# Optimization experiments

Measured on AMD Instinct MI355X. Metric: run time of the kernel, lower is better.

Reference implementation:

```python
import jax, jax.numpy as jnp
import numpy as np

B, N, H, ITERS = 4, 4096, 128, 8
EPS = 1e-5  # torch LayerNorm default


def _mlp(x, w1, b1, w2, b2, w3, b3):
    x = jax.nn.relu(x @ w1.T + b1)
    x = jax.nn.relu(x @ w2.T + b2)
    return x @ w3.T + b3


def setup_inputs() -> dict:
    key = jax.random.key(0)
    ks = jax.random.split(key, 16)
    s = 0.05
    nrm = lambda k, shape: jax.random.normal(k, shape, jnp.float32) * s
    z = lambda *shape: jnp.zeros(shape, jnp.float32)
    return {
        "x": jax.random.normal(ks[0], (B, N, N), jnp.float32),
        "k": jax.random.uniform(ks[1], (B,), jnp.float32, 1.0, 10.0),
        "n": jax.random.uniform(ks[2], (B,), jnp.float32, 10.0, 100.0),
        "mask": (jax.random.uniform(ks[3], (B, N)) < 0.9).astype(jnp.float32),
        # init MLP: 2 -> H -> H -> H (torch Linear convention: [out, in])
        "init_w1": nrm(ks[4], (H, 2)), "init_b1": z(H),
        "init_w2": nrm(ks[5], (H, H)), "init_b2": z(H),
        "init_w3": nrm(ks[6], (H, H)), "init_b3": z(H),
        # msg MLP: H -> H -> H -> H
        "msg_w1": nrm(ks[7], (H, H)), "msg_b1": z(H),
        "msg_w2": nrm(ks[8], (H, H)), "msg_b2": z(H),
        "msg_w3": nrm(ks[9], (H, H)), "msg_b3": z(H),
        # LSTMCell (gate order i, f, g, o)
        "lstm_wih": nrm(ks[10], (4 * H, H)), "lstm_whh": nrm(ks[11], (4 * H, H)),
        "lstm_bih": z(4 * H), "lstm_bhh": z(4 * H),
        # LayerNorm affine
        "ln_g": jnp.ones(H, jnp.float32), "ln_b": z(H),
        # vote MLP: H -> H -> H -> 1
        "vote_w1": nrm(ks[12], (H, H)), "vote_b1": z(H),
        "vote_w2": nrm(ks[13], (H, H)), "vote_b2": z(H),
        "vote_w3": nrm(ks[14], (1, H)), "vote_b3": z(1),
    }


def reference(x, k, n, mask,
              init_w1, init_b1, init_w2, init_b2, init_w3, init_b3,
              msg_w1, msg_b1, msg_w2, msg_b2, msg_w3, msg_b3,
              lstm_wih, lstm_whh, lstm_bih, lstm_bhh,
              ln_g, ln_b,
              vote_w1, vote_b1, vote_w2, vote_b2, vote_w3, vote_b3):
    b, n_node, _ = x.shape

    def ln(h):
        mu = h.mean(-1, keepdims=True)
        xc = h - mu
        var = (xc * xc).mean(-1, keepdims=True)
        return xc * jax.lax.rsqrt(var + EPS) * ln_g + ln_b

    nk = jnp.stack([k, n], axis=1)                          # [B, 2]
    init0 = _mlp(nk, init_w1, init_b1, init_w2, init_b2, init_w3, init_b3)
    h = jnp.broadcast_to(init0[:, None, :], (b, n_node, init0.shape[-1]))  # [B, N, H]
    c = jnp.zeros_like(h)
    embed = ln(h)
    for _ in range(ITERS):
        m = _mlp(embed, msg_w1, msg_b1, msg_w2, msg_b2, msg_w3, msg_b3)   # [B, N, H]
        msg = jnp.einsum('bij,bjh->bih', x, m)                            # dense aggregation
        gates = msg @ lstm_wih.T + lstm_bih + h @ lstm_whh.T + lstm_bhh   # [B, N, 4H]
        i, f, g, o = jnp.split(gates, 4, axis=-1)
        c = jax.nn.sigmoid(f) * c + jax.nn.sigmoid(i) * jnp.tanh(g)
        h = jax.nn.sigmoid(o) * jnp.tanh(c)
        embed = ln(h)
    vote = _mlp(embed, vote_w1, vote_b1, vote_w2, vote_b2, vote_w3, vote_b3)[..., 0]  # [B, N]
    return jax.nn.sigmoid((vote * mask).sum(axis=1))        # [B]
```

## Files before the change

kernel.cpp:

```cpp
#include <hip/hip_runtime.h>
#include <cstddef>
#include <cstdint>

#define LN_EPS 1e-5f

typedef __attribute__((ext_vector_type(8))) short bf16x8;
typedef __attribute__((ext_vector_type(4))) float f32x4;

__device__ __forceinline__ unsigned short f2bf(float f) {
    unsigned u = __float_as_uint(f);
    u += 0x7FFFu + ((u >> 16) & 1u);
    return (unsigned short)(u >> 16);
}
__device__ __forceinline__ float bf2f(unsigned short s) {
    return __uint_as_float(((unsigned)s) << 16);
}
__device__ __forceinline__ float sigf(float x) { return 1.f / (1.f + __expf(-x)); }

__device__ __forceinline__ void gload_lds16(const void* g, void* l) {
    __builtin_amdgcn_global_load_lds(
        (const __attribute__((address_space(1))) unsigned int*)(unsigned long long)(uintptr_t)g,
        (__attribute__((address_space(3))) unsigned int*)(unsigned int)(uintptr_t)l,
        16, 0, 0);
}

__device__ __forceinline__ void layer128(const unsigned short* __restrict__ W,
                                         const bf16x8 a[4], f32x4 acc[8],
                                         int lr, int lq)
{
#pragma unroll
    for (int s = 0; s < 4; ++s) {
#pragma unroll
        for (int tn = 0; tn < 8; ++tn) {
            bf16x8 b = *(const bf16x8*)(W + (tn * 16 + lr) * 128 + s * 32 + lq * 8);
            acc[tn] = __builtin_amdgcn_mfma_f32_16x16x32_bf16(a[s], b, acc[tn], 0, 0, 0);
        }
    }
}

template<bool FP8>
__global__ __launch_bounds__(256)
void msg_mlp_kernel(const unsigned short* __restrict__ embed,
                    const unsigned short* __restrict__ w1, const float* __restrict__ b1,
                    const unsigned short* __restrict__ w2, const float* __restrict__ b2,
                    const unsigned short* __restrict__ w3, const float* __restrict__ b3,
                    unsigned short* __restrict__ m_t, unsigned char* __restrict__ m8,
                    int N)
{
    __shared__ unsigned short sact[4][16][136];
    const int lane = threadIdx.x & 63, wave = threadIdx.x >> 6;
    const int lr = lane & 15, lq = lane >> 4;
    const int r0 = (blockIdx.x * 4 + wave) * 16;

    bf16x8 a[4];
    f32x4 acc[8];

#pragma unroll
    for (int s = 0; s < 4; ++s)
        a[s] = *(const bf16x8*)(embed + (long long)(r0 + lr) * 128 + s * 32 + lq * 8);
#pragma unroll
    for (int tn = 0; tn < 8; ++tn) acc[tn] = (f32x4)(0.f);
    layer128(w1, a, acc, lr, lq);

#pragma unroll
    for (int tn = 0; tn < 8; ++tn) {
        float bb = b1[tn * 16 + lr];
#pragma unroll
        for (int r = 0; r < 4; ++r) {
            float v = acc[tn][r] + bb; v = v > 0.f ? v : 0.f;
            sact[wave][lq * 4 + r][tn * 16 + lr] = f2bf(v);
        }
    }
    __syncthreads();
#pragma unroll
    for (int s = 0; s < 4; ++s)
        a[s] = *(const bf16x8*)&sact[wave][lr][s * 32 + lq * 8];
#pragma unroll
    for (int tn = 0; tn < 8; ++tn) acc[tn] = (f32x4)(0.f);
    layer128(w2, a, acc, lr, lq);

#pragma unroll
    for (int tn = 0; tn < 8; ++tn) {
        float bb = b2[tn * 16 + lr];
#pragma unroll
        for (int r = 0; r < 4; ++r) {
            float v = acc[tn][r] + bb; v = v > 0.f ? v : 0.f;
            sact[wave][lq * 4 + r][tn * 16 + lr] = f2bf(v);
        }
    }
    __syncthreads();
#pragma unroll
    for (int s = 0; s < 4; ++s)
        a[s] = *(const bf16x8*)&sact[wave][lr][s * 32 + lq * 8];
#pragma unroll
    for (int tn = 0; tn < 8; ++tn) acc[tn] = (f32x4)(0.f);
    layer128(w3, a, acc, lr, lq);

    const int batch = r0 / N;
    const int rin0 = r0 - batch * N + lq * 4;
#pragma unroll
    for (int tn = 0; tn < 8; ++tn) {
        float bb = b3[tn * 16 + lr];
        float v0 = acc[tn][0] + bb, v1 = acc[tn][1] + bb;
        float v2 = acc[tn][2] + bb, v3 = acc[tn][3] + bb;
        if constexpr (FP8) {
            int pk = __builtin_amdgcn_cvt_pk_fp8_f32(v0, v1, 0, false);
            pk = __builtin_amdgcn_cvt_pk_fp8_f32(v2, v3, pk, true);
            *(unsigned int*)(m8 + (long long)(batch * 128 + tn * 16 + lr) * N + rin0) = (unsigned)pk;
        } else {
            ushort4 o;
            o.x = f2bf(v0); o.y = f2bf(v1); o.z = f2bf(v2); o.w = f2bf(v3);
            *(ushort4*)(m_t + ((long long)(batch * 128 + tn * 16 + lr)) * N + rin0) = o;
        }
    }
}

__global__ __launch_bounds__(256)
void agg_fp8_kernel(const unsigned char* __restrict__ x8,
                    const unsigned char* __restrict__ m8,
                    unsigned short* __restrict__ msgp, int N, long long BNH)
{
    __shared__ unsigned char sA[2][128 * 128];
    __shared__ unsigned char sB[2][128 * 128];

    const int tid = threadIdx.x;
    const int lane = tid & 63, w = tid >> 6;
    const int lr = lane & 15, lq = lane >> 4;
    const int wr = w & 1, wc = w >> 1;
    const int r0 = blockIdx.x * 128;
    const int ksp = blockIdx.y;
    const int batch = blockIdx.z;
    const int kbase = ksp * (N >> 2);
    const int nsteps = (N >> 2) >> 7;

    const unsigned char* xrow = x8 + (long long)batch * N * N;
    const unsigned char* mrow = m8 + (long long)batch * 128 * N;

    f32x4 acc[4][4];
#pragma unroll
    for (int tr = 0; tr < 4; ++tr)
#pragma unroll
        for (int tn = 0; tn < 4; ++tn) acc[tr][tn] = (f32x4)(0.f);

    auto stage = [&](int b, int step) {
        const int k0 = kbase + step * 128;
#pragma unroll
        for (int j = 0; j < 4; ++j) {
            const int c = ((w * 4 + j) << 6) + lane;
            const int row = c >> 3;
            const int gs = (c & 7) ^ (row & 7);
            gload_lds16(xrow + (long long)(r0 + row) * N + k0 + gs * 16,
                        (char*)sA[b] + (w * 4 + j) * 1024);
        }
#pragma unroll
        for (int j = 0; j < 4; ++j) {
            const int c = ((w * 4 + j) << 6) + lane;
            const int row = c >> 3;
            const int gs = (c & 7) ^ (row & 7);
            gload_lds16(mrow + (long long)row * N + k0 + gs * 16,
                        (char*)sB[b] + (w * 4 + j) * 1024);
        }
    };

    stage(0, 0);
    __syncthreads();
    int buf = 0;
    for (int step = 0; step < nsteps; ++step) {
        if (step + 1 < nsteps) stage(buf ^ 1, step + 1);
        const unsigned char* A  = sA[buf];
        const unsigned char* Bp = sB[buf];
#pragma unroll
        for (int ks = 0; ks < 4; ++ks) {
            const int g    = ks * 4 + lq;
            const int half = (g & 1) << 3;
            const int s16  = g >> 1;
            long af[4], bfr[4];
#pragma unroll
            for (int tr = 0; tr < 4; ++tr) {
                const int row = wr * 64 + tr * 16 + lr;
                af[tr] = *(const long*)(A + row * 128 + ((s16 ^ (row & 7)) << 4) + half);
            }
#pragma unroll
            for (int tn = 0; tn < 4; ++tn) {
                const int row = wc * 64 + tn * 16 + lr;
                bfr[tn] = *(const long*)(Bp + row * 128 + ((s16 ^ (row & 7)) << 4) + half);
            }
#pragma unroll
            for (int tr = 0; tr < 4; ++tr)
#pragma unroll
                for (int tn = 0; tn < 4; ++tn)
                    acc[tr][tn] = __builtin_amdgcn_mfma_f32_16x16x32_fp8_fp8(
                        af[tr], bfr[tn], acc[tr][tn], 0, 0, 0);
        }
        __syncthreads();
        buf ^= 1;
    }

    unsigned short* outb = msgp + (long long)ksp * BNH + (long long)(batch * N + r0) * 128;
#pragma unroll
    for (int tr = 0; tr < 4; ++tr)
#pragma unroll
        for (int tn = 0; tn < 4; ++tn)
#pragma unroll
            for (int r = 0; r < 4; ++r)
                outb[(long long)(wr * 64 + tr * 16 + lq * 4 + r) * 128 + wc * 64 + tn * 16 + lr]
                    = f2bf(acc[tr][tn][r]);
}

__global__ __launch_bounds__(256)
void agg_fallback_kernel(const float* __restrict__ xf,
                         const unsigned short* __restrict__ mt, float* __restrict__ msgp0,
                         int N)
{
    __shared__ float sacc[4][16][132];
    const int lane = threadIdx.x & 63, wave = threadIdx.x >> 6;
    const int lr = lane & 15, lq = lane >> 4;
    const int batch = blockIdx.y;
    const int rowBase = blockIdx.x * 16;
    const int kBase = wave * (N >> 2);
    const int kIters = N >> 7;

    const float* af = xf + (long long)batch * N * N + (long long)(rowBase + lr) * N + kBase + lq * 8;
    const long long bbase = (long long)batch * 128 * N + (long long)lr * N + kBase + lq * 8;

    f32x4 acc[8];
#pragma unroll
    for (int tn = 0; tn < 8; ++tn) acc[tn] = (f32x4)(0.f);

    for (int it = 0; it < kIters; ++it) {
        const int k = it * 32;
        float4 lo = *(const float4*)(af + k);
        float4 hi = *(const float4*)(af + k + 4);
        bf16x8 a0;
        a0[0] = (short)f2bf(lo.x); a0[1] = (short)f2bf(lo.y);
        a0[2] = (short)f2bf(lo.z); a0[3] = (short)f2bf(lo.w);
        a0[4] = (short)f2bf(hi.x); a0[5] = (short)f2bf(hi.y);
        a0[6] = (short)f2bf(hi.z); a0[7] = (short)f2bf(hi.w);
#pragma unroll
        for (int tn = 0; tn < 8; ++tn) {
            bf16x8 b0 = *(const bf16x8*)(mt + bbase + (long long)tn * 16 * N + k);
            acc[tn] = __builtin_amdgcn_mfma_f32_16x16x32_bf16(a0, b0, acc[tn], 0, 0, 0);
        }
    }

#pragma unroll
    for (int tn = 0; tn < 8; ++tn)
#pragma unroll
        for (int r = 0; r < 4; ++r)
            sacc[wave][lq * 4 + r][tn * 16 + lr] = acc[tn][r];
    __syncthreads();
    {
        const int t = threadIdx.x;
        const int row = t >> 4, cb2 = (t & 15) * 8;
        float o[8];
#pragma unroll
        for (int j = 0; j < 8; ++j)
            o[j] = sacc[0][row][cb2 + j] + sacc[1][row][cb2 + j]
                 + sacc[2][row][cb2 + j] + sacc[3][row][cb2 + j];
        float* dst = msgp0 + (long long)(batch * N + rowBase + row) * 128 + cb2;
        *(float4*)dst = make_float4(o[0], o[1], o[2], o[3]);
        *(float4*)(dst + 4) = make_float4(o[4], o[5], o[6], o[7]);
    }
}

template<int NPART, bool BF16P>
__global__ __launch_bounds__(256)
void gates_lstm_kernel(const void* __restrict__ msgp, long long BNH,
                       unsigned short* hb, float* cb,
                       const unsigned short* __restrict__ wih,
                       const unsigned short* __restrict__ whh,
                       const float* __restrict__ bih, const float* __restrict__ bhh,
                       const float* __restrict__ lng, const float* __restrict__ lnb,
                       unsigned short* __restrict__ embed_out)
{
    __shared__ float sred[4][16][2];
    const int lane = threadIdx.x & 63, wave = threadIdx.x >> 6;
    const int lr = lane & 15, lq = lane >> 4;
    const int r0 = blockIdx.x * 16;

    f32x4 acc[8];
#pragma unroll
    for (int t = 0; t < 8; ++t) acc[t] = (f32x4)(0.f);

    bf16x8 a[4];
#pragma unroll
    for (int s = 0; s < 4; ++s) {
        const long long base = (long long)(r0 + lr) * 128 + s * 32 + lq * 8;
        float v[8];
        if constexpr (BF16P) {
            const unsigned short* mp = (const unsigned short*)msgp;
            bf16x8 t0 = *(const bf16x8*)(mp + base);
#pragma unroll
            for (int e = 0; e < 8; ++e) v[e] = bf2f((unsigned short)t0[e]);
#pragma unroll
            for (int j = 1; j < NPART; ++j) {
                bf16x8 tj = *(const bf16x8*)(mp + (long long)j * BNH + base);
#pragma unroll
                for (int e = 0; e < 8; ++e) v[e] += bf2f((unsigned short)tj[e]);
            }
        } else {
            const float* mp = (const float*)msgp;
            float4 t0 = *(const float4*)(mp + base);
            float4 t1 = *(const float4*)(mp + base + 4);
            v[0] = t0.x; v[1] = t0.y; v[2] = t0.z; v[3] = t0.w;
            v[4] = t1.x; v[5] = t1.y; v[6] = t1.z; v[7] = t1.w;
#pragma unroll
            for (int j = 1; j < NPART; ++j) {
                float4 u0 = *(const float4*)(mp + (long long)j * BNH + base);
                float4 u1 = *(const float4*)(mp + (long long)j * BNH + base + 4);
                v[0] += u0.x; v[1] += u0.y; v[2] += u0.z; v[3] += u0.w;
                v[4] += u1.x; v[5] += u1.y; v[6] += u1.z; v[7] += u1.w;
            }
        }
        bf16x8 r8;
#pragma unroll
        for (int e = 0; e < 8; ++e) r8[e] = (short)f2bf(v[e]);
        a[s] = r8;
    }
#pragma unroll
    for (int s = 0; s < 4; ++s)
#pragma unroll
        for (int tt = 0; tt < 8; ++tt) {
            const int brow = (tt >> 1) * 128 + wave * 32 + (tt & 1) * 16 + lr;
            bf16x8 b = *(const bf16x8*)(wih + brow * 128 + s * 32 + lq * 8);
            acc[tt] = __builtin_amdgcn_mfma_f32_16x16x32_bf16(a[s], b, acc[tt], 0, 0, 0);
        }
#pragma unroll
    for (int s = 0; s < 4; ++s)
        a[s] = *(const bf16x8*)((const unsigned short*)hb + (long long)(r0 + lr) * 128 + s * 32 + lq * 8);
#pragma unroll
    for (int s = 0; s < 4; ++s)
#pragma unroll
        for (int tt = 0; tt < 8; ++tt) {
            const int brow = (tt >> 1) * 128 + wave * 32 + (tt & 1) * 16 + lr;
            bf16x8 b = *(const bf16x8*)(whh + brow * 128 + s * 32 + lq * 8);
            acc[tt] = __builtin_amdgcn_mfma_f32_16x16x32_bf16(a[s], b, acc[tt], 0, 0, 0);
        }

    float hn[2][4];
    float4* cw = (float4*)cb;
#pragma unroll
    for (int half = 0; half < 2; ++half) {
        const int col = wave * 32 + half * 16 + lr;
        const float bi  = bih[col]       + bhh[col];
        const float bf_ = bih[col + 128] + bhh[col + 128];
        const float bg  = bih[col + 256] + bhh[col + 256];
        const float bo  = bih[col + 384] + bhh[col + 384];
        const long long cidx = ((long long)blockIdx.x * 8 + wave * 2 + half) * 64 + lane;
        float4 cold = cw[cidx];
        float co[4] = {cold.x, cold.y, cold.z, cold.w};
        float cn[4];
#pragma unroll
        for (int r = 0; r < 4; ++r) {
            float iv = acc[0 + half][r] + bi;
            float fv = acc[2 + half][r] + bf_;
            float gv = acc[4 + half][r] + bg;
            float ov = acc[6 + half][r] + bo;
            float cc = sigf(fv) * co[r] + sigf(iv) * tanhf(gv);
            cn[r] = cc;
            hn[half][r] = sigf(ov) * tanhf(cc);
        }
        float4 cnew = {cn[0], cn[1], cn[2], cn[3]};
        cw[cidx] = cnew;
    }

    float ps1[4], ps2[4];
#pragma unroll
    for (int r = 0; r < 4; ++r) {
        float s1 = hn[0][r] + hn[1][r];
        float s2 = hn[0][r] * hn[0][r] + hn[1][r] * hn[1][r];
#pragma unroll
        for (int m = 1; m <= 8; m <<= 1) {
            s1 += __shfl_xor(s1, m);
            s2 += __shfl_xor(s2, m);
        }
        ps1[r] = s1; ps2[r] = s2;
    }
    if (lr == 0) {
#pragma unroll
        for (int r = 0; r < 4; ++r) {
            sred[wave][lq * 4 + r][0] = ps1[r];
            sred[wave][lq * 4 + r][1] = ps2[r];
        }
    }
    __syncthreads();

#pragma unroll
    for (int half = 0; half < 2; ++half) {
        const int col = wave * 32 + half * 16 + lr;
        const float g = lng[col], bb = lnb[col];
#pragma unroll
        for (int r = 0; r < 4; ++r) {
            const int row = lq * 4 + r;
            float S1 = sred[0][row][0] + sred[1][row][0] + sred[2][row][0] + sred[3][row][0];
            float S2 = sred[0][row][1] + sred[1][row][1] + sred[2][row][1] + sred[3][row][1];
            float mean = S1 * (1.f / 128.f);
            float var  = S2 * (1.f / 128.f) - mean * mean;
            float rs = rsqrtf(var + LN_EPS);
            long long off = (long long)(r0 + row) * 128 + col;
            hb[off] = f2bf(hn[half][r]);
            embed_out[off] = f2bf((hn[half][r] - mean) * rs * g + bb);
        }
    }
}

__global__ __launch_bounds__(256)
void vote_mlp_kernel(const unsigned short* __restrict__ embed,
                     const unsigned short* __restrict__ w1, const float* __restrict__ b1,
                     const unsigned short* __restrict__ w2, const float* __restrict__ b2,
                     const float* __restrict__ w3, const float* __restrict__ b3p,
                     const float* __restrict__ mask, float* __restrict__ logit, int N)
{
    __shared__ unsigned short sact[4][16][136];
    const int lane = threadIdx.x & 63, wave = threadIdx.x >> 6;
    const int lr = lane & 15, lq = lane >> 4;
    const int r0 = (blockIdx.x * 4 + wave) * 16;

    bf16x8 a[4];
    f32x4 acc[8];
#pragma unroll
    for (int s = 0; s < 4; ++s)
        a[s] = *(const bf16x8*)(embed + (long long)(r0 + lr) * 128 + s * 32 + lq * 8);
#pragma unroll
    for (int tn = 0; tn < 8; ++tn) acc[tn] = (f32x4)(0.f);
    layer128(w1, a, acc, lr, lq);

#pragma unroll
    for (int tn = 0; tn < 8; ++tn) {
        float bb = b1[tn * 16 + lr];
#pragma unroll
        for (int r = 0; r < 4; ++r) {
            float v = acc[tn][r] + bb; v = v > 0.f ? v : 0.f;
            sact[wave][lq * 4 + r][tn * 16 + lr] = f2bf(v);
        }
    }
    __syncthreads();
#pragma unroll
    for (int s = 0; s < 4; ++s)
        a[s] = *(const bf16x8*)&sact[wave][lr][s * 32 + lq * 8];
#pragma unroll
    for (int tn = 0; tn < 8; ++tn) acc[tn] = (f32x4)(0.f);
    layer128(w2, a, acc, lr, lq);

    float dot[4] = {0.f, 0.f, 0.f, 0.f};
#pragma unroll
    for (int tn = 0; tn < 8; ++tn) {
        const int col = tn * 16 + lr;
        const float bb = b2[col], w3c = w3[col];
#pragma unroll
        for (int r = 0; r < 4; ++r) {
            float v = acc[tn][r] + bb; v = v > 0.f ? v : 0.f;
            dot[r] += v * w3c;
        }
    }
#pragma unroll
    for (int r = 0; r < 4; ++r)
#pragma unroll
        for (int m = 1; m <= 8; m <<= 1) dot[r] += __shfl_xor(dot[r], m);

    const int batch = r0 / N;
    const float b3 = b3p[0];
    const int base = r0 + lq * 4;
    float wsum = mask[base + 0] * (dot[0] + b3) + mask[base + 1] * (dot[1] + b3)
               + mask[base + 2] * (dot[2] + b3) + mask[base + 3] * (dot[3] + b3);
    float t = (lr == 0) ? wsum : 0.f;
    t += __shfl_xor(t, 16);
    t += __shfl_xor(t, 32);
    if (lane == 0) atomicAdd(&logit[batch], t);
}

__global__ __launch_bounds__(128)
void init_kernel(const float* __restrict__ kk, const float* __restrict__ nn,
                 const float* __restrict__ w1, const float* __restrict__ b1,
                 const float* __restrict__ w2, const float* __restrict__ b2,
                 const float* __restrict__ w3, const float* __restrict__ b3,
                 const float* __restrict__ lng, const float* __restrict__ lnb,
                 float* __restrict__ init0, float* __restrict__ embed0,
                 float* __restrict__ logit, int H)
{
    int b = blockIdx.x, j = threadIdx.x;
    __shared__ float s1[128];
    __shared__ float s2[128];
    __shared__ float red[128];
    if (j == 0) logit[b] = 0.f;
    float kv = kk[b], nv = nn[b];
    float h1 = w1[j * 2 + 0] * kv + w1[j * 2 + 1] * nv + b1[j];
    h1 = h1 > 0.f ? h1 : 0.f;
    s1[j] = h1; __syncthreads();
    float h2 = b2[j];
    for (int q = 0; q < H; ++q) h2 += w2[j * H + q] * s1[q];
    h2 = h2 > 0.f ? h2 : 0.f;
    s2[j] = h2; __syncthreads();
    float o = b3[j];
    for (int q = 0; q < H; ++q) o += w3[j * H + q] * s2[q];
    init0[b * H + j] = o;

    red[j] = o; __syncthreads();
    for (int s = 64; s > 0; s >>= 1) { if (j < s) red[j] += red[j + s]; __syncthreads(); }
    float mu = red[0] / (float)H;
    __syncthreads();
    float d = o - mu;
    red[j] = d * d; __syncthreads();
    for (int s = 64; s > 0; s >>= 1) { if (j < s) red[j] += red[j + s]; __syncthreads(); }
    float var = red[0] / (float)H;
    embed0[b * H + j] = d * rsqrtf(var + LN_EPS) * lng[j] + lnb[j];
}

__global__ void bcast_kernel(const float* __restrict__ init0, const float* __restrict__ embed0,
                             unsigned short* __restrict__ hb, float* __restrict__ cb,
                             unsigned short* __restrict__ embed,
                             long long total, long long NH)
{
    long long idx = (long long)blockIdx.x * blockDim.x + threadIdx.x;
    if (idx >= total) return;
    int b = (int)(idx / NH);
    int j = (int)(idx & 127);
    hb[idx] = f2bf(init0[b * 128 + j]);
    embed[idx] = f2bf(embed0[b * 128 + j]);
    cb[idx] = 0.f;
}

__global__ void cast8_kernel(const float* __restrict__ x, unsigned char* __restrict__ x8,
                             long long n8)
{
    long long i = ((long long)blockIdx.x * blockDim.x + threadIdx.x);
    if (i >= n8) return;
    const float* s = x + i * 8;
    float4 a = *(const float4*)s;
    float4 b = *(const float4*)(s + 4);
    int lo = __builtin_amdgcn_cvt_pk_fp8_f32(a.x, a.y, 0, false);
    lo = __builtin_amdgcn_cvt_pk_fp8_f32(a.z, a.w, lo, true);
    int hi = __builtin_amdgcn_cvt_pk_fp8_f32(b.x, b.y, 0, false);
    hi = __builtin_amdgcn_cvt_pk_fp8_f32(b.z, b.w, hi, true);
    int2 o; o.x = lo; o.y = hi;
    *(int2*)(x8 + i * 8) = o;
}

struct CastArgs {
    const float* src[7];
    unsigned short* dst[7];
    int n[7];
};

__global__ void castw_kernel(CastArgs a)
{
    int rg = blockIdx.y;
    int i = (blockIdx.x * blockDim.x + threadIdx.x) * 4;
    if (i < a.n[rg]) {
        float4 v = *(const float4*)(a.src[rg] + i);
        ushort4 o;
        o.x = f2bf(v.x); o.y = f2bf(v.y); o.z = f2bf(v.z); o.w = f2bf(v.w);
        *(ushort4*)(a.dst[rg] + i) = o;
    }
}

__global__ void sigmoid_kernel(const float* __restrict__ logit, float* __restrict__ out, int B)
{
    int b = threadIdx.x;
    if (b < B) out[b] = 1.f / (1.f + __expf(-logit[b]));
}

extern "C" void kernel_launch(void* const* d_in, const int* in_sizes, int n_in,
                              void* d_out, int out_size, void* d_ws, size_t ws_size,
                              hipStream_t stream)
{
    const float* x    = (const float*)d_in[0];
    const float* kk   = (const float*)d_in[1];
    const float* nn   = (const float*)d_in[2];
    const float* mask = (const float*)d_in[3];
    const float* iw1  = (const float*)d_in[4];
    const float* ib1  = (const float*)d_in[5];
    const float* iw2  = (const float*)d_in[6];
    const float* ib2  = (const float*)d_in[7];
    const float* iw3  = (const float*)d_in[8];
    const float* ib3  = (const float*)d_in[9];
    const float* mw1  = (const float*)d_in[10];
    const float* mb1  = (const float*)d_in[11];
    const float* mw2  = (const float*)d_in[12];
    const float* mb2  = (const float*)d_in[13];
    const float* mw3  = (const float*)d_in[14];
    const float* mb3  = (const float*)d_in[15];
    const float* wih  = (const float*)d_in[16];
    const float* whh  = (const float*)d_in[17];
    const float* bih  = (const float*)d_in[18];
    const float* bhh  = (const float*)d_in[19];
    const float* lng  = (const float*)d_in[20];
    const float* lnb  = (const float*)d_in[21];
    const float* vw1  = (const float*)d_in[22];
    const float* vb1  = (const float*)d_in[23];
    const float* vw2  = (const float*)d_in[24];
    const float* vb2  = (const float*)d_in[25];
    const float* vw3  = (const float*)d_in[26];
    const float* vb3  = (const float*)d_in[27];
    float* out = (float*)d_out;

    const int B = in_sizes[1];
    const int H = in_sizes[5];
    const int N = in_sizes[3] / B;
    const long long NH  = (long long)N * H;
    const long long BNH = (long long)B * NH;
    const int M = B * N;

    char* p = (char*)d_ws;
    auto alloc = [&](long long bytes) {
        char* q = p; p += (bytes + 255) & ~255LL; return q;
    };
    float*          cb     = (float*)alloc(BNH * 4);
    unsigned short* embed  = (unsigned short*)alloc(BNH * 2);
    unsigned short* hb     = (unsigned short*)alloc(BNH * 2);
    unsigned short* m_t    = (unsigned short*)alloc(BNH * 2);
    unsigned short* msgp   = (unsigned short*)alloc(4 * BNH * 2);
    float*          init0  = (float*)alloc((long long)B * H * 4);
    float*          embed0 = (float*)alloc((long long)B * H * 4);
    float*          logit  = (float*)alloc((long long)B * 4);
    unsigned short* wb_m1  = (unsigned short*)alloc((long long)H * H * 2);
    unsigned short* wb_m2  = (unsigned short*)alloc((long long)H * H * 2);
    unsigned short* wb_m3  = (unsigned short*)alloc((long long)H * H * 2);
    unsigned short* wb_ih  = (unsigned short*)alloc(4LL * H * H * 2);
    unsigned short* wb_hh  = (unsigned short*)alloc(4LL * H * H * 2);
    unsigned short* wb_v1  = (unsigned short*)alloc((long long)H * H * 2);
    unsigned short* wb_v2  = (unsigned short*)alloc((long long)H * H * 2);
    unsigned char*  m8_t   = (unsigned char*)alloc(BNH);
    unsigned char*  x8     = (unsigned char*)alloc((long long)B * N * N);
    const bool use_x8 = ((long long)(p - (char*)d_ws) <= (long long)ws_size);

    init_kernel<<<B, H, 0, stream>>>(kk, nn, iw1, ib1, iw2, ib2, iw3, ib3, lng, lnb,
                                     init0, embed0, logit, H);
    {
        long long nb = (BNH + 255) / 256;
        bcast_kernel<<<dim3((unsigned)nb), 256, 0, stream>>>(init0, embed0, hb, cb, embed, BNH, NH);
    }
    {
        CastArgs ca;
        ca.src[0] = mw1; ca.dst[0] = wb_m1; ca.n[0] = H * H;
        ca.src[1] = mw2; ca.dst[1] = wb_m2; ca.n[1] = H * H;
        ca.src[2] = mw3; ca.dst[2] = wb_m3; ca.n[2] = H * H;
        ca.src[3] = wih; ca.dst[3] = wb_ih; ca.n[3] = 4 * H * H;
        ca.src[4] = whh; ca.dst[4] = wb_hh; ca.n[4] = 4 * H * H;
        ca.src[5] = vw1; ca.dst[5] = wb_v1; ca.n[5] = H * H;
        ca.src[6] = vw2; ca.dst[6] = wb_v2; ca.n[6] = H * H;
        castw_kernel<<<dim3(64, 7), 256, 0, stream>>>(ca);
    }
    if (use_x8) {
        long long n8 = (long long)B * N * N / 8;
        cast8_kernel<<<dim3((unsigned)((n8 + 255) / 256)), 256, 0, stream>>>(x, x8, n8);
    }

    dim3 gridRow(M / 64);
    dim3 gridRow16(M / 16);
    dim3 gridAggNew(N / 128, 4, B);
    dim3 gridAggOld(N / 16, B);

    for (int it = 0; it < 8; ++it) {
        if (use_x8) {
            msg_mlp_kernel<true><<<gridRow, 256, 0, stream>>>(embed, wb_m1, mb1, wb_m2, mb2,
                                                              wb_m3, mb3, m_t, m8_t, N);
            agg_fp8_kernel<<<gridAggNew, 256, 0, stream>>>(x8, m8_t, msgp, N, BNH);
            gates_lstm_kernel<4, true><<<gridRow16, 256, 0, stream>>>(
                (const void*)msgp, BNH, hb, cb, wb_ih, wb_hh, bih, bhh, lng, lnb, embed);
        } else {
            msg_mlp_kernel<false><<<gridRow, 256, 0, stream>>>(embed, wb_m1, mb1, wb_m2, mb2,
                                                               wb_m3, mb3, m_t, m8_t, N);
            agg_fallback_kernel<<<gridAggOld, 256, 0, stream>>>(x, m_t, (float*)msgp, N);
            gates_lstm_kernel<1, false><<<gridRow16, 256, 0, stream>>>(
                (const void*)msgp, BNH, hb, cb, wb_ih, wb_hh, bih, bhh, lng, lnb, embed);
        }
    }

    vote_mlp_kernel<<<gridRow, 256, 0, stream>>>(embed, wb_v1, vb1, wb_v2, vb2,
                                                 vw3, vb3, mask, logit, N);
    sigmoid_kernel<<<1, 64, 0, stream>>>(logit, out, B);
}
```

Measured before the change: 1.135 ms.

## Fuse whole pipeline into one persistent cooperative kernel with grid syncs

Replaces the sequence of per-iteration kernel launches (msg MLP, fp8 aggregation, gates/LSTM, vote) with a single cooperative kernel of 512 blocks that runs all phases separated by grid-wide barriers. The message MLP is fused into the gates tile so the new embedding stays in shared memory instead of round-tripping through global memory. The vote MLP is fused into the final gates pass in the same way. This removes launch overhead and some intermediate traffic. In exchange the aggregation loses its double-buffered LDS prefetch, and each phase pays for grid sync costs.

```diff
diff --git a/kernel.cpp b/kernel.cpp
--- a/kernel.cpp
+++ b/kernel.cpp
@@ -1,8 +1,13 @@
 #include <hip/hip_runtime.h>
+#include <hip/hip_cooperative_groups.h>
 #include <cstddef>
 #include <cstdint>
 
+namespace cg = cooperative_groups;
+
 #define LN_EPS 1e-5f
+#define NB 512
+#define NT 256
 
 typedef __attribute__((ext_vector_type(8))) short bf16x8;
 typedef __attribute__((ext_vector_type(4))) float f32x4;
@@ -22,6 +27,537 @@
         (const __attribute__((address_space(1))) unsigned int*)(unsigned long long)(uintptr_t)g,
         (__attribute__((address_space(3))) unsigned int*)(unsigned int)(uintptr_t)l,
         16, 0, 0);
+}
+
+struct UberArgs {
+    const float *x, *kk, *nn, *mask;
+    const float *iw1, *ib1, *iw2, *ib2, *iw3, *ib3;
+    const float *mw1, *mb1, *mw2, *mb2, *mw3, *mb3;
+    const float *wih, *whh, *bih, *bhh, *lng, *lnb;
+    const float *vw1, *vb1, *vw2, *vb2, *vw3, *vb3;
+    unsigned short *wm1, *wm2, *wm3, *wih_b, *whh_b, *wv1, *wv2;
+    unsigned char *x8, *m8;
+    unsigned short *msgp;
+    unsigned short *hb;
+    float *cb;
+    float *init0, *embed0, *logit, *out;
+    int N, B, iters;
+    long long BNH;
+};
+
+__device__ void prologue(const UberArgs& A, char* smem)
+{
+    const int tid = threadIdx.x;
+    const long long gtid = (long long)blockIdx.x * NT + tid;
+    const long long GT = (long long)NB * NT;
+    const int N = A.N, B_ = A.B;
+
+    const long long n8 = (long long)B_ * N * N / 8;
+    for (long long i = gtid; i < n8; i += GT) {
+        const float* s = A.x + i * 8;
+        float4 a0 = *(const float4*)s;
+        float4 b0 = *(const float4*)(s + 4);
+        int lo = __builtin_amdgcn_cvt_pk_fp8_f32(a0.x, a0.y, 0, false);
+        lo = __builtin_amdgcn_cvt_pk_fp8_f32(a0.z, a0.w, lo, true);
+        int hi = __builtin_amdgcn_cvt_pk_fp8_f32(b0.x, b0.y, 0, false);
+        hi = __builtin_amdgcn_cvt_pk_fp8_f32(b0.z, b0.w, hi, true);
+        int2 o; o.x = lo; o.y = hi;
+        *(int2*)(A.x8 + i * 8) = o;
+    }
+    {
+        const float* srcs[7] = {A.mw1, A.mw2, A.mw3, A.wih, A.whh, A.vw1, A.vw2};
+        unsigned short* dsts[7] = {A.wm1, A.wm2, A.wm3, A.wih_b, A.whh_b, A.wv1, A.wv2};
+        const int ns[7] = {16384, 16384, 16384, 65536, 65536, 16384, 16384};
+        for (int rg = 0; rg < 7; ++rg) {
+            const float* s = srcs[rg]; unsigned short* d = dsts[rg];
+            const int n4 = ns[rg] >> 2;
+            for (long long i = gtid; i < n4; i += GT) {
+                float4 v = *(const float4*)(s + i * 4);
+                ushort4 o;
+                o.x = f2bf(v.x); o.y = f2bf(v.y); o.z = f2bf(v.z); o.w = f2bf(v.w);
+                *(ushort4*)(d + i * 4) = o;
+            }
+        }
+    }
+    const long long nc4 = A.BNH >> 2;
+    const float4 z4 = make_float4(0.f, 0.f, 0.f, 0.f);
+    for (long long i = gtid; i < nc4; i += GT) ((float4*)A.cb)[i] = z4;
+    if (blockIdx.x == 0 && tid < B_) A.logit[tid] = 0.f;
+
+    if ((int)blockIdx.x >= NB - B_) {
+        const int b = blockIdx.x - (NB - B_);
+        float* s1 = (float*)smem;
+        float* s2 = s1 + 128;
+        float* red = s2 + 128;
+        const bool act = tid < 128;
+        const int j = tid;
+        const float kv = A.kk[b], nv = A.nn[b];
+        float h1 = 0.f, h2 = 0.f, o = 0.f;
+        if (act) {
+            h1 = A.iw1[j * 2 + 0] * kv + A.iw1[j * 2 + 1] * nv + A.ib1[j];
+            h1 = h1 > 0.f ? h1 : 0.f;
+            s1[j] = h1;
+        }
+        __syncthreads();
+        if (act) {
+            h2 = A.ib2[j];
+            for (int q = 0; q < 128; ++q) h2 += A.iw2[j * 128 + q] * s1[q];
+            h2 = h2 > 0.f ? h2 : 0.f;
+            s2[j] = h2;
+        }
+        __syncthreads();
+        if (act) {
+            o = A.ib3[j];
+            for (int q = 0; q < 128; ++q) o += A.iw3[j * 128 + q] * s2[q];
+            A.init0[b * 128 + j] = o;
+            red[j] = o;
+        }
+        __syncthreads();
+        for (int s = 64; s > 0; s >>= 1) { if (tid < s) red[tid] += red[tid + s]; __syncthreads(); }
+        const float mu = red[0] * (1.f / 128.f);
+        __syncthreads();
+        if (act) red[j] = (o - mu) * (o - mu);
+        __syncthreads();
+        for (int s = 64; s > 0; s >>= 1) { if (tid < s) red[tid] += red[tid + s]; __syncthreads(); }
+        if (act) {
+            const float var = red[0] * (1.f / 128.f);
+            A.embed0[b * 128 + j] = (o - mu) * rsqrtf(var + LN_EPS) * A.lng[j] + A.lnb[j];
+        }
+    }
+}
+
+__device__ __forceinline__ void msg_tile(const UberArgs& A, int tile,
+                                         unsigned short (*ebt)[136], unsigned short (*act)[136])
+{
+    const int tid = threadIdx.x;
+    const int lane = tid & 63, wave = tid >> 6;
+    const int lr = lane & 15, lq = lane >> 4;
+    const int r0 = tile * 16;
+    const int N = A.N;
+    bf16x8 a[4];
+    f32x4 acc2[2];
+
+#pragma unroll
+    for (int s = 0; s < 4; ++s) a[s] = *(const bf16x8*)&ebt[lr][s * 32 + lq * 8];
+    acc2[0] = (f32x4)(0.f); acc2[1] = (f32x4)(0.f);
+#pragma unroll
+    for (int s = 0; s < 4; ++s)
+#pragma unroll
+        for (int t = 0; t < 2; ++t) {
+            const int orow = wave * 32 + t * 16 + lr;
+            bf16x8 b = *(const bf16x8*)(A.wm1 + orow * 128 + s * 32 + lq * 8);
+            acc2[t] = __builtin_amdgcn_mfma_f32_16x16x32_bf16(a[s], b, acc2[t], 0, 0, 0);
+        }
+#pragma unroll
+    for (int t = 0; t < 2; ++t) {
+        const int col = wave * 32 + t * 16 + lr;
+        const float bb = A.mb1[col];
+#pragma unroll
+        for (int r = 0; r < 4; ++r) {
+            float v = acc2[t][r] + bb; v = v > 0.f ? v : 0.f;
+            act[lq * 4 + r][col] = f2bf(v);
+        }
+    }
+    __syncthreads();
+#pragma unroll
+    for (int s = 0; s < 4; ++s) a[s] = *(const bf16x8*)&act[lr][s * 32 + lq * 8];
+    acc2[0] = (f32x4)(0.f); acc2[1] = (f32x4)(0.f);
+#pragma unroll
+    for (int s = 0; s < 4; ++s)
+#pragma unroll
+        for (int t = 0; t < 2; ++t) {
+            const int orow = wave * 32 + t * 16 + lr;
+            bf16x8 b = *(const bf16x8*)(A.wm2 + orow * 128 + s * 32 + lq * 8);
+            acc2[t] = __builtin_amdgcn_mfma_f32_16x16x32_bf16(a[s], b, acc2[t], 0, 0, 0);
+        }
+    __syncthreads();
+#pragma unroll
+    for (int t = 0; t < 2; ++t) {
+        const int col = wave * 32 + t * 16 + lr;
+        const float bb = A.mb2[col];
+#pragma unroll
+        for (int r = 0; r < 4; ++r) {
+            float v = acc2[t][r] + bb; v = v > 0.f ? v : 0.f;
+            ebt[lq * 4 + r][col] = f2bf(v);
+        }
+    }
+    __syncthreads();
+#pragma unroll
+    for (int s = 0; s < 4; ++s) a[s] = *(const bf16x8*)&ebt[lr][s * 32 + lq * 8];
+    acc2[0] = (f32x4)(0.f); acc2[1] = (f32x4)(0.f);
+#pragma unroll
+    for (int s = 0; s < 4; ++s)
+#pragma unroll
+        for (int t = 0; t < 2; ++t) {
+            const int orow = wave * 32 + t * 16 + lr;
+            bf16x8 b = *(const bf16x8*)(A.wm3 + orow * 128 + s * 32 + lq * 8);
+            acc2[t] = __builtin_amdgcn_mfma_f32_16x16x32_bf16(a[s], b, acc2[t], 0, 0, 0);
+        }
+    const int batch = r0 / N;
+    const int rin0 = r0 - batch * N + lq * 4;
+#pragma unroll
+    for (int t = 0; t < 2; ++t) {
+        const int col = wave * 32 + t * 16 + lr;
+        const float bb = A.mb3[col];
+        float v0 = acc2[t][0] + bb, v1 = acc2[t][1] + bb;
+        float v2 = acc2[t][2] + bb, v3 = acc2[t][3] + bb;
+        int pk = __builtin_amdgcn_cvt_pk_fp8_f32(v0, v1, 0, false);
+        pk = __builtin_amdgcn_cvt_pk_fp8_f32(v2, v3, pk, true);
+        *(unsigned int*)(A.m8 + (long long)(batch * 128 + col) * N + rin0) = (unsigned)pk;
+    }
+}
+
+__device__ __forceinline__ void vote_tile(const UberArgs& A, int tile,
+                                          unsigned short (*ebt)[136], unsigned short (*act)[136],
+                                          float* sdot)
+{
+    const int tid = threadIdx.x;
+    const int lane = tid & 63, wave = tid >> 6;
+    const int lr = lane & 15, lq = lane >> 4;
+    const int r0 = tile * 16;
+    const int N = A.N;
+    bf16x8 a[4];
+    f32x4 acc2[2];
+
+#pragma unroll
+    for (int s = 0; s < 4; ++s) a[s] = *(const bf16x8*)&ebt[lr][s * 32 + lq * 8];
+    acc2[0] = (f32x4)(0.f); acc2[1] = (f32x4)(0.f);
+#pragma unroll
+    for (int s = 0; s < 4; ++s)
+#pragma unroll
+        for (int t = 0; t < 2; ++t) {
+            const int orow = wave * 32 + t * 16 + lr;
+            bf16x8 b = *(const bf16x8*)(A.wv1 + orow * 128 + s * 32 + lq * 8);
+            acc2[t] = __builtin_amdgcn_mfma_f32_16x16x32_bf16(a[s], b, acc2[t], 0, 0, 0);
+        }
+#pragma unroll
+    for (int t = 0; t < 2; ++t) {
+        const int col = wave * 32 + t * 16 + lr;
+        const float bb = A.vb1[col];
+#pragma unroll
+        for (int r = 0; r < 4; ++r) {
+            float v = acc2[t][r] + bb; v = v > 0.f ? v : 0.f;
+            act[lq * 4 + r][col] = f2bf(v);
+        }
+    }
+    __syncthreads();
+#pragma unroll
+    for (int s = 0; s < 4; ++s) a[s] = *(const bf16x8*)&act[lr][s * 32 + lq * 8];
+    acc2[0] = (f32x4)(0.f); acc2[1] = (f32x4)(0.f);
+#pragma unroll
+    for (int s = 0; s < 4; ++s)
+#pragma unroll
+        for (int t = 0; t < 2; ++t) {
+            const int orow = wave * 32 + t * 16 + lr;
+            bf16x8 b = *(const bf16x8*)(A.wv2 + orow * 128 + s * 32 + lq * 8);
+            acc2[t] = __builtin_amdgcn_mfma_f32_16x16x32_bf16(a[s], b, acc2[t], 0, 0, 0);
+        }
+    float dot[4] = {0.f, 0.f, 0.f, 0.f};
+#pragma unroll
+    for (int t = 0; t < 2; ++t) {
+        const int col = wave * 32 + t * 16 + lr;
+        const float bb = A.vb2[col], w3c = A.vw3[col];
+#pragma unroll
+        for (int r = 0; r < 4; ++r) {
+            float v = acc2[t][r] + bb; v = v > 0.f ? v : 0.f;
+            dot[r] += v * w3c;
+        }
+    }
+#pragma unroll
+    for (int r = 0; r < 4; ++r)
+#pragma unroll
+        for (int m = 1; m <= 8; m <<= 1) dot[r] += __shfl_xor(dot[r], m);
+    if (lr == 0) {
+#pragma unroll
+        for (int r = 0; r < 4; ++r) sdot[wave * 16 + lq * 4 + r] = dot[r];
+    }
+    __syncthreads();
+    if (wave == 0) {
+        const int batch = r0 / N;
+        const int rin = r0 - batch * N + lr;
+        float s = sdot[lr] + sdot[16 + lr] + sdot[32 + lr] + sdot[48 + lr];
+        float val = (s + A.vb3[0]) * A.mask[batch * N + rin];
+#pragma unroll
+        for (int m = 1; m <= 8; m <<= 1) val += __shfl_xor(val, m);
+        if (lane == 0) atomicAdd(&A.logit[batch], val);
+    }
+    __syncthreads();
+}
+
+__device__ __forceinline__ void gates_tile(const UberArgs& A, int tile,
+                                           unsigned short (*ebt)[136], float* sred)
+{
+    const int tid = threadIdx.x;
+    const int lane = tid & 63, wave = tid >> 6;
+    const int lr = lane & 15, lq = lane >> 4;
+    const int r0 = tile * 16;
+    const long long BNH = A.BNH;
+
+    f32x4 acc[8];
+#pragma unroll
+    for (int t = 0; t < 8; ++t) acc[t] = (f32x4)(0.f);
+
+    bf16x8 a[4];
+#pragma unroll
+    for (int s = 0; s < 4; ++s) {
+        const long long base = (long long)(r0 + lr) * 128 + s * 32 + lq * 8;
+        float v[8];
+        bf16x8 t0 = *(const bf16x8*)(A.msgp + base);
+#pragma unroll
+        for (int e = 0; e < 8; ++e) v[e] = bf2f((unsigned short)t0[e]);
+#pragma unroll
+        for (int j = 1; j < 4; ++j) {
+            bf16x8 tj = *(const bf16x8*)(A.msgp + (long long)j * BNH + base);
+#pragma unroll
+            for (int e = 0; e < 8; ++e) v[e] += bf2f((unsigned short)tj[e]);
+        }
+        bf16x8 r8;
+#pragma unroll
+        for (int e = 0; e < 8; ++e) r8[e] = (short)f2bf(v[e]);
+        a[s] = r8;
+    }
+#pragma unroll
+    for (int s = 0; s < 4; ++s)
+#pragma unroll
+        for (int tt = 0; tt < 8; ++tt) {
+            const int brow = (tt >> 1) * 128 + wave * 32 + (tt & 1) * 16 + lr;
+            bf16x8 b = *(const bf16x8*)(A.wih_b + brow * 128 + s * 32 + lq * 8);
+            acc[tt] = __builtin_amdgcn_mfma_f32_16x16x32_bf16(a[s], b, acc[tt], 0, 0, 0);
+        }
+#pragma unroll
+    for (int s = 0; s < 4; ++s)
+        a[s] = *(const bf16x8*)(A.hb + (long long)(r0 + lr) * 128 + s * 32 + lq * 8);
+#pragma unroll
+    for (int s = 0; s < 4; ++s)
+#pragma unroll
+        for (int tt = 0; tt < 8; ++tt) {
+            const int brow = (tt >> 1) * 128 + wave * 32 + (tt & 1) * 16 + lr;
+            bf16x8 b = *(const bf16x8*)(A.whh_b + brow * 128 + s * 32 + lq * 8);
+            acc[tt] = __builtin_amdgcn_mfma_f32_16x16x32_bf16(a[s], b, acc[tt], 0, 0, 0);
+        }
+
+    float hn[2][4];
+    float4* cw = (float4*)A.cb;
+#pragma unroll
+    for (int half = 0; half < 2; ++half) {
+        const int col = wave * 32 + half * 16 + lr;
+        const float bi  = A.bih[col]       + A.bhh[col];
+        const float bf_ = A.bih[col + 128] + A.bhh[col + 128];
+        const float bg  = A.bih[col + 256] + A.bhh[col + 256];
+        const float bo  = A.bih[col + 384] + A.bhh[col + 384];
+        const long long cidx = ((long long)tile * 8 + wave * 2 + half) * 64 + lane;
+        float4 cold = cw[cidx];
+        float co[4] = {cold.x, cold.y, cold.z, cold.w};
+        float cn[4];
+#pragma unroll
+        for (int r = 0; r < 4; ++r) {
+            float iv = acc[0 + half][r] + bi;
+            float fv = acc[2 + half][r] + bf_;
+            float gv = acc[4 + half][r] + bg;
+            float ov = acc[6 + half][r] + bo;
+            float cc = sigf(fv) * co[r] + sigf(iv) * tanhf(gv);
+            cn[r] = cc;
+            hn[half][r] = sigf(ov) * tanhf(cc);
+        }
+        cw[cidx] = make_float4(cn[0], cn[1], cn[2], cn[3]);
+    }
+
+    float ps1[4], ps2[4];
+#pragma unroll
+    for (int r = 0; r < 4; ++r) {
+        float s1 = hn[0][r] + hn[1][r];
+        float s2 = hn[0][r] * hn[0][r] + hn[1][r] * hn[1][r];
+#pragma unroll
+        for (int m = 1; m <= 8; m <<= 1) {
+            s1 += __shfl_xor(s1, m);
+            s2 += __shfl_xor(s2, m);
+        }
+        ps1[r] = s1; ps2[r] = s2;
+    }
+    if (lr == 0) {
+#pragma unroll
+        for (int r = 0; r < 4; ++r) {
+            sred[(wave * 16 + lq * 4 + r) * 2 + 0] = ps1[r];
+            sred[(wave * 16 + lq * 4 + r) * 2 + 1] = ps2[r];
+        }
+    }
+    __syncthreads();
+
+#pragma unroll
+    for (int half = 0; half < 2; ++half) {
+        const int col = wave * 32 + half * 16 + lr;
+        const float g = A.lng[col], bb = A.lnb[col];
+#pragma unroll
+        for (int r = 0; r < 4; ++r) {
+            const int row = lq * 4 + r;
+            float S1 = sred[(row) * 2] + sred[(16 + row) * 2] + sred[(32 + row) * 2] + sred[(48 + row) * 2];
+            float S2 = sred[(row) * 2 + 1] + sred[(16 + row) * 2 + 1] + sred[(32 + row) * 2 + 1] + sred[(48 + row) * 2 + 1];
+            float mean = S1 * (1.f / 128.f);
+            float var  = S2 * (1.f / 128.f) - mean * mean;
+            float rs = rsqrtf(var + LN_EPS);
+            A.hb[(long long)(r0 + row) * 128 + col] = f2bf(hn[half][r]);
+            ebt[row][col] = f2bf((hn[half][r] - mean) * rs * g + bb);
+        }
+    }
+}
+
+__device__ void agg_phase(const UberArgs& A, char* smem)
+{
+    unsigned char* sA = (unsigned char*)smem;
+    unsigned char* sB = (unsigned char*)smem + 16384;
+
+    const int tid = threadIdx.x;
+    const int lane = tid & 63, w = tid >> 6;
+    const int lr = lane & 15, lq = lane >> 4;
+    const int wr = w & 1, wc = w >> 1;
+    const int N = A.N;
+    const int nrt = N >> 7;
+    const int bid = blockIdx.x;
+    const int xt    = bid % nrt;
+    const int ksp   = (bid / nrt) & 3;
+    const int batch = bid / (nrt * 4);
+    const int r0 = xt * 128;
+    const int kbase = ksp * (N >> 2);
+    const int nsteps = (N >> 2) >> 7;
+
+    const unsigned char* xrow = A.x8 + (long long)batch * N * N;
+    const unsigned char* mrow = A.m8 + (long long)batch * 128 * N;
+
+    f32x4 acc[4][4];
+#pragma unroll
+    for (int tr = 0; tr < 4; ++tr)
+#pragma unroll
+        for (int tn = 0; tn < 4; ++tn) acc[tr][tn] = (f32x4)(0.f);
+
+    for (int step = 0; step < nsteps; ++step) {
+        const int k0 = kbase + step * 128;
+#pragma unroll
+        for (int j = 0; j < 4; ++j) {
+            const int c = ((w * 4 + j) << 6) + lane;
+            const int row = c >> 3;
+            const int gs = (c & 7) ^ (row & 7);
+            gload_lds16(xrow + (long long)(r0 + row) * N + k0 + gs * 16,
+                        sA + (w * 4 + j) * 1024);
+        }
+#pragma unroll
+        for (int j = 0; j < 4; ++j) {
+            const int c = ((w * 4 + j) << 6) + lane;
+            const int row = c >> 3;
+            const int gs = (c & 7) ^ (row & 7);
+            gload_lds16(mrow + (long long)row * N + k0 + gs * 16,
+                        sB + (w * 4 + j) * 1024);
+        }
+        __syncthreads();
+#pragma unroll
+        for (int ks = 0; ks < 4; ++ks) {
+            const int g    = ks * 4 + lq;
+            const int half = (g & 1) << 3;
+            const int s16  = g >> 1;
+            long af[4], bfr[4];
+#pragma unroll
+            for (int tr = 0; tr < 4; ++tr) {
+                const int row = wr * 64 + tr * 16 + lr;
+                af[tr] = *(const long*)(sA + row * 128 + ((s16 ^ (row & 7)) << 4) + half);
+            }
+#pragma unroll
+            for (int tn = 0; tn < 4; ++tn) {
+                const int row = wc * 64 + tn * 16 + lr;
+                bfr[tn] = *(const long*)(sB + row * 128 + ((s16 ^ (row & 7)) << 4) + half);
+            }
+#pragma unroll
+            for (int tr = 0; tr < 4; ++tr)
+#pragma unroll
+                for (int tn = 0; tn < 4; ++tn)
+                    acc[tr][tn] = __builtin_amdgcn_mfma_f32_16x16x32_fp8_fp8(
+                        af[tr], bfr[tn], acc[tr][tn], 0, 0, 0);
+        }
+        __syncthreads();
+    }
+
+    unsigned short* outb = A.msgp + (long long)ksp * A.BNH + (long long)(batch * N + r0) * 128;
+#pragma unroll
+    for (int tr = 0; tr < 4; ++tr)
+#pragma unroll
+        for (int tn = 0; tn < 4; ++tn)
+#pragma unroll
+            for (int r = 0; r < 4; ++r)
+                outb[(long long)(wr * 64 + tr * 16 + lq * 4 + r) * 128 + wc * 64 + tn * 16 + lr]
+                    = f2bf(acc[tr][tn][r]);
+}
+
+__device__ void phase1(const UberArgs& A, char* smem)
+{
+    const int tid = threadIdx.x;
+    const long long gtid = (long long)blockIdx.x * NT + tid;
+    const long long GT = (long long)NB * NT;
+    const long long NH = (long long)A.N * 128;
+
+    const long long n4 = A.BNH >> 2;
+    for (long long i = gtid; i < n4; i += GT) {
+        const long long idx = i * 4;
+        const int b = (int)(idx / NH);
+        const int j = (int)(idx & 127);
+        ushort4 o;
+        o.x = f2bf(A.init0[b * 128 + j]);
+        o.y = f2bf(A.init0[b * 128 + j + 1]);
+        o.z = f2bf(A.init0[b * 128 + j + 2]);
+        o.w = f2bf(A.init0[b * 128 + j + 3]);
+        ((ushort4*)A.hb)[i] = o;
+    }
+
+    unsigned short (*ebt)[136] = (unsigned short(*)[136])smem;
+    unsigned short (*act)[136] = (unsigned short(*)[136])(smem + 4352);
+    const int ntiles = (A.B * A.N) / 16;
+    for (int pass = 0; pass < ntiles / NB; ++pass) {
+        const int tile = blockIdx.x + pass * NB;
+        const int batch = (tile * 16) / A.N;
+        __syncthreads();
+        for (int i = tid; i < 16 * 128; i += NT) {
+            const int row = i >> 7, col = i & 127;
+            ebt[row][col] = f2bf(A.embed0[batch * 128 + col]);
+        }
+        __syncthreads();
+        msg_tile(A, tile, ebt, act);
+        __syncthreads();
+    }
+}
+
+__device__ void g_phase(const UberArgs& A, char* smem, bool do_vote)
+{
+    unsigned short (*ebt)[136] = (unsigned short(*)[136])smem;
+    unsigned short (*act)[136] = (unsigned short(*)[136])(smem + 4352);
+    float* sred = (float*)(smem + 8704);
+    float* sdot = (float*)(smem + 9472);
+    const int ntiles = (A.B * A.N) / 16;
+    for (int pass = 0; pass < ntiles / NB; ++pass) {
+        const int tile = blockIdx.x + pass * NB;
+        __syncthreads();
+        gates_tile(A, tile, ebt, sred);
+        __syncthreads();
+        if (do_vote) vote_tile(A, tile, ebt, act, sdot);
+        else         msg_tile(A, tile, ebt, act);
+        __syncthreads();
+    }
+}
+
+__global__ __launch_bounds__(NT, 2)
+void uber_kernel(UberArgs A)
+{
+    __shared__ __align__(16) char smem[32768];
+    cg::grid_group grid = cg::this_grid();
+
+    prologue(A, smem);
+    __threadfence(); grid.sync();
+    phase1(A, smem);
+    __threadfence(); grid.sync();
+    for (int it = 0; it < A.iters; ++it) {
+        agg_phase(A, smem);
+        __threadfence(); grid.sync();
+        g_phase(A, smem, it == A.iters - 1);
+        __threadfence(); grid.sync();
+    }
+    if (blockIdx.x == 0 && threadIdx.x < (unsigned)A.B)
+        A.out[threadIdx.x] = sigf(A.logit[threadIdx.x]);
 }
 
 __device__ __forceinline__ void layer128(const unsigned short* __restrict__ W,
@@ -167,8 +703,8 @@
     int buf = 0;
     for (int step = 0; step < nsteps; ++step) {
         if (step + 1 < nsteps) stage(buf ^ 1, step + 1);
-        const unsigned char* A  = sA[buf];
-        const unsigned char* Bp = sB[buf];
+        const unsigned char* Ab = sA[buf];
+        const unsigned char* Bb = sB[buf];
 #pragma unroll
         for (int ks = 0; ks < 4; ++ks) {
             const int g    = ks * 4 + lq;
@@ -178,12 +714,12 @@
 #pragma unroll
             for (int tr = 0; tr < 4; ++tr) {
                 const int row = wr * 64 + tr * 16 + lr;
-                af[tr] = *(const long*)(A + row * 128 + ((s16 ^ (row & 7)) << 4) + half);
+                af[tr] = *(const long*)(Ab + row * 128 + ((s16 ^ (row & 7)) << 4) + half);
             }
 #pragma unroll
             for (int tn = 0; tn < 4; ++tn) {
                 const int row = wc * 64 + tn * 16 + lr;
-                bfr[tn] = *(const long*)(Bp + row * 128 + ((s16 ^ (row & 7)) << 4) + half);
+                bfr[tn] = *(const long*)(Bb + row * 128 + ((s16 ^ (row & 7)) << 4) + half);
             }
 #pragma unroll
             for (int tr = 0; tr < 4; ++tr)
@@ -360,8 +896,7 @@
             cn[r] = cc;
             hn[half][r] = sigf(ov) * tanhf(cc);
         }
-        float4 cnew = {cn[0], cn[1], cn[2], cn[3]};
-        cw[cidx] = cnew;
+        cw[cidx] = make_float4(cn[0], cn[1], cn[2], cn[3]);
     }
 
     float ps1[4], ps2[4];
@@ -622,7 +1157,27 @@
     unsigned short* wb_v2  = (unsigned short*)alloc((long long)H * H * 2);
     unsigned char*  m8_t   = (unsigned char*)alloc(BNH);
     unsigned char*  x8     = (unsigned char*)alloc((long long)B * N * N);
-    const bool use_x8 = ((long long)(p - (char*)d_ws) <= (long long)ws_size);
+    const bool ws_ok = ((long long)(p - (char*)d_ws) <= (long long)ws_size);
+    const bool coop_shape = ws_ok && B == 4 && N == 4096 && H == 128;
+
+    if (coop_shape) {
+        UberArgs ua;
+        ua.x = x; ua.kk = kk; ua.nn = nn; ua.mask = mask;
+        ua.iw1 = iw1; ua.ib1 = ib1; ua.iw2 = iw2; ua.ib2 = ib2; ua.iw3 = iw3; ua.ib3 = ib3;
+        ua.mw1 = mw1; ua.mb1 = mb1; ua.mw2 = mw2; ua.mb2 = mb2; ua.mw3 = mw3; ua.mb3 = mb3;
+        ua.wih = wih; ua.whh = whh; ua.bih = bih; ua.bhh = bhh; ua.lng = lng; ua.lnb = lnb;
+        ua.vw1 = vw1; ua.vb1 = vb1; ua.vw2 = vw2; ua.vb2 = vb2; ua.vw3 = vw3; ua.vb3 = vb3;
+        ua.wm1 = wb_m1; ua.wm2 = wb_m2; ua.wm3 = wb_m3;
+        ua.wih_b = wb_ih; ua.whh_b = wb_hh; ua.wv1 = wb_v1; ua.wv2 = wb_v2;
+        ua.x8 = x8; ua.m8 = m8_t; ua.msgp = msgp; ua.hb = hb; ua.cb = cb;
+        ua.init0 = init0; ua.embed0 = embed0; ua.logit = logit; ua.out = out;
+        ua.N = N; ua.B = B; ua.iters = 8; ua.BNH = BNH;
+        void* args[] = { &ua };
+        hipError_t e = hipLaunchCooperativeKernel((const void*)uber_kernel, dim3(NB), dim3(NT),
+                                                  args, 0, stream);
+        if (e == hipSuccess) return;
+        (void)hipGetLastError();
+    }
 
     init_kernel<<<B, H, 0, stream>>>(kk, nn, iw1, ib1, iw2, ib2, iw3, ib3, lng, lnb,
                                      init0, embed0, logit, H);
@@ -641,7 +1196,7 @@
         ca.src[6] = vw2; ca.dst[6] = wb_v2; ca.n[6] = H * H;
         castw_kernel<<<dim3(64, 7), 256, 0, stream>>>(ca);
     }
-    if (use_x8) {
+    if (ws_ok) {
         long long n8 = (long long)B * N * N / 8;
         cast8_kernel<<<dim3((unsigned)((n8 + 255) / 256)), 256, 0, stream>>>(x, x8, n8);
     }
@@ -652,7 +1207,7 @@
     dim3 gridAggOld(N / 16, B);
 
     for (int it = 0; it < 8; ++it) {
-        if (use_x8) {
+        if (ws_ok) {
             msg_mlp_kernel<true><<<gridRow, 256, 0, stream>>>(embed, wb_m1, mb1, wb_m2, mb2,
                                                               wb_m3, mb3, m_t, m8_t, N);
             agg_fp8_kernel<<<gridAggNew, 256, 0, stream>>>(x8, m8_t, msgp, N, BNH);
```

After: 3.149 ms. 2.77x slower.
